# Kernel optimization log

Measured on AMD Instinct MI355X. Metric: run time of the kernel, lower is better.

## Reference

```python
import jax, jax.numpy as jnp
import numpy as np


def cv_sigmoid(z):
    # split sigmoid: sigmoid(Re) + i*sigmoid(Im)
    return jax.nn.sigmoid(z.real) + 1j * jax.nn.sigmoid(z.imag)


def cv_polar_tanh(z):
    # tanh on magnitude, phase preserved: tanh(|z|) * z / |z|
    mag = jnp.abs(z)
    safe = jnp.where(mag == 0, 1.0, mag)
    return (jnp.tanh(mag) / safe).astype(z.dtype) * z


def setup_inputs() -> dict:
    key = jax.random.key(0)
    B, D, H = 16384, 512, 512
    ks = jax.random.split(key, 12)
    names = ['x_re', 'x_im', 'h_re', 'h_im', 'Wx_re', 'Wx_im', 'Wh_re', 'Wh_im', 'bx_re', 'bx_im', 'bh_re', 'bh_im']
    shapes = [(B, D), (B, D), (B, H), (B, H), (3, H, D), (3, H, D), (3, H, H), (3, H, H), (3, H), (3, H), (3, H), (3, H)]
    out = {}
    for n, s, k in zip(names, shapes, ks):
        scale = 1.0 if n[0] in ('x', 'h') else (1.0 / np.sqrt(s[-1]))
        out[n] = jax.random.normal(k, s, dtype=jnp.float32) * scale
    return out


def reference(x_re, x_im, h_re, h_im, Wx_re, Wx_im, Wh_re, Wh_im, bx_re, bx_im, bh_re, bh_im):
    x = (x_re + 1j * x_im).astype(jnp.complex64)   # [B, D]
    h = (h_re + 1j * h_im).astype(jnp.complex64)   # [B, H]
    Wx = (Wx_re + 1j * Wx_im).astype(jnp.complex64)  # [3, H, D] (z, r, h)
    Wh = (Wh_re + 1j * Wh_im).astype(jnp.complex64)  # [3, H, H]
    bx = (bx_re + 1j * bx_im).astype(jnp.complex64)  # [3, H]
    bh = (bh_re + 1j * bh_im).astype(jnp.complex64)  # [3, H]

    # input projections for all three gates at once: [3, B, H]
    px = jnp.einsum('bd,khd->kbh', x, Wx) + bx[:, None, :]
    # hidden projections for z and r gates
    pz = jnp.einsum('bh,gh->bg', h, Wh[0]) + bh[0]
    pr = jnp.einsum('bh,gh->bg', h, Wh[1]) + bh[1]

    z = cv_sigmoid(px[0] + pz)
    r = cv_sigmoid(px[1] + pr)

    ph = jnp.einsum('bh,gh->bg', r * h, Wh[2]) + bh[2]
    h_tilde = cv_polar_tanh(px[2] + ph)

    h_new = (1.0 - z) * h + z * h_tilde  # [B, H] complex
    # return as stacked real/imag float tensor [B, H, 2]
    return jnp.stack([h_new.real, h_new.imag], axis=-1)
```

## Files before the change

### kernel.cpp

```cpp
#include <hip/hip_runtime.h>
#include <hip/hip_bf16.h>

typedef __bf16 bf16_t;
typedef __bf16 bf16x8 __attribute__((ext_vector_type(8)));
typedef __bf16 bf16x4 __attribute__((ext_vector_type(4)));
typedef float f32x4 __attribute__((ext_vector_type(4)));


__device__ __forceinline__ void gl_lds16(const bf16_t* g, bf16_t* l) {
  __builtin_amdgcn_global_load_lds(
      (const __attribute__((address_space(1))) void*)g,
      (__attribute__((address_space(3))) void*)l, 16, 0, 0);
}

__device__ __forceinline__ float fast_sigmoid(float x) {
  return 1.0f / (1.0f + __expf(-x));
}

__global__ void pack_A(const float* __restrict__ x_re, const float* __restrict__ x_im,
                       const float* __restrict__ h_re, const float* __restrict__ h_im,
                       bf16_t* __restrict__ A) {
  int q = blockIdx.x * blockDim.x + threadIdx.x;
  int i4 = q << 2;
  int b = i4 >> 11;
  int k = i4 & 2047;
  int seg = k >> 9;
  int off = k & 511;
  const float* s = (seg == 0) ? x_re : (seg == 1) ? x_im : (seg == 2) ? h_re : h_im;
  const float4 v = *(const float4*)(s + (size_t)b * 512 + off);
  bf16x4 o = { (bf16_t)v.x, (bf16_t)v.y, (bf16_t)v.z, (bf16_t)v.w };
  *(bf16x4*)(A + (size_t)b * 2048 + k) = o;
}

__global__ void pack_W(const float* __restrict__ Wx_re, const float* __restrict__ Wx_im,
                       const float* __restrict__ Wh_re, const float* __restrict__ Wh_im,
                       bf16_t* __restrict__ W1t, bf16_t* __restrict__ W2t) {
  int q = blockIdx.x * blockDim.x + threadIdx.x;
  int n, k2, g, j, p;
  const float *Wre, *Wim;
  bf16_t* dst;
  if (q < 1048576) {
    n = q >> 9; k2 = (q & 511) << 2;
    g = n >> 10; j = (n & 1023) >> 1; p = n & 1;
    int pair = k2 >> 10;
    Wre = pair ? Wh_re : Wx_re;
    Wim = pair ? Wh_im : Wx_im;
    dst = W1t + (size_t)n * 2048 + k2;
  } else if (q < 1048576 + 262144) {
    int q2 = q - 1048576;
    n = 2048 + (q2 >> 8); k2 = (q2 & 255) << 2;
    g = 2; j = (n - 2048) >> 1; p = n & 1;
    Wre = Wx_re; Wim = Wx_im;
    dst = W1t + (size_t)n * 2048 + k2;
  } else {
    int q3 = q - (1048576 + 262144);
    n = q3 >> 8; k2 = (q3 & 255) << 2;
    g = 2; j = n >> 1; p = n & 1;
    Wre = Wh_re; Wim = Wh_im;
    dst = W2t + (size_t)n * 1024 + k2;
  }
  int klocal = k2 & 1023;
  int half = klocal >> 9;
  int off = klocal & 511;
  size_t sidx = ((size_t)g * 512 + j) * 512 + off;
  const float* s = (half == 0) ? (p ? Wim : Wre) : (p ? Wre : Wim);
  float sgn = (half == 1 && p == 0) ? -1.0f : 1.0f;
  float4 v = *(const float4*)(s + sidx);
  bf16x4 o = { (bf16_t)(sgn * v.x), (bf16_t)(sgn * v.y),
               (bf16_t)(sgn * v.z), (bf16_t)(sgn * v.w) };
  *(bf16x4*)dst = o;
}

template <int MODE>
__launch_bounds__(512, 2)
__global__ void gemm_fused(const bf16_t* __restrict__ A, const bf16_t* __restrict__ W,
                           int LDA, int LDW,
                           bf16_t* __restrict__ zbuf, bf16_t* __restrict__ A2,
                           float* __restrict__ outbuf,
                           const float* __restrict__ h_re, const float* __restrict__ h_im,
                           const float* __restrict__ bx_re, const float* __restrict__ bx_im,
                           const float* __restrict__ bh_re, const float* __restrict__ bh_im) {
  __shared__ __align__(16) bf16_t As[2][256 * 64];
  __shared__ __align__(16) bf16_t Bs[2][256 * 64];

  const int bid = blockIdx.x;
  const int xcd = bid & 7;
  const int idx = bid >> 3;
  const int ntile = idx >> 3;
  const int mtile = (xcd << 3) + (idx & 7);
  const int m0 = mtile * 256;
  const int n0 = ntile * 256;
  const int region = (MODE == 1) ? (ntile >> 2) : 0;
  const int KEND = (MODE == 1) ? ((region < 2) ? 2048 : 1024) : 1024;
  const int nKT = KEND >> 6;

  const int tid = threadIdx.x;
  const int lane = tid & 63;
  const int w = tid >> 6;
  const int wr = w >> 2;
  const int wc = w & 3;

  const int rb = tid >> 3;
  const int cc = tid & 7;
  const int cs = cc ^ (rb & 7);
  const bf16_t* Ag = A + (size_t)(m0 + rb) * LDA + cs * 8;
  const bf16_t* Wg = W + (size_t)(n0 + rb) * LDW + cs * 8;

#define STAGE_A(s, bufi, kt2) \
  gl_lds16(Ag + (size_t)(s) * 64 * LDA + (kt2) * 64, &As[bufi][tid * 8 + (s) * 4096])
#define STAGE_B(s, bufi, kt2) \
  gl_lds16(Wg + (size_t)(s) * 64 * LDW + (kt2) * 64, &Bs[bufi][tid * 8 + (s) * 4096])

  const int quad = lane >> 4, lrow = lane & 15;
  int aOff[8], bOff[4];
#pragma unroll
  for (int mt = 0; mt < 8; ++mt) {
    const int r = wr * 128 + mt * 16 + lrow;
    aOff[mt] = r * 64 + ((quad ^ (r & 7)) << 3);
  }
#pragma unroll
  for (int nt = 0; nt < 4; ++nt) {
    const int r = wc * 64 + nt * 16 + lrow;
    bOff[nt] = r * 64 + ((quad ^ (r & 7)) << 3);
  }

  f32x4 acc[8][4] = {};

#pragma unroll
  for (int s = 0; s < 4; ++s) STAGE_A(s, 0, 0);
#pragma unroll
  for (int s = 0; s < 4; ++s) STAGE_B(s, 0, 0);
  STAGE_A(0, 1, 1);
  STAGE_A(2, 1, 1);
  asm volatile("s_waitcnt vmcnt(2)" ::: "memory");
  __builtin_amdgcn_s_barrier();

  for (int kt = 0; kt < nKT; ++kt) {
    const int b = kt & 1;
    const bf16_t* Ab = As[b];
    const bf16_t* Bb = Bs[b];
    const bool s1 = (kt + 1 < nKT);
    const bool s2 = (kt + 2 < nKT);

    bf16x8 bk0[4], bk1[4], aA[4], aB[4], aC[4], aD[4];

#pragma unroll
    for (int nt = 0; nt < 4; ++nt) bk0[nt] = *(const bf16x8*)(Bb + bOff[nt]);
#pragma unroll
    for (int i = 0; i < 4; ++i) aA[i] = *(const bf16x8*)(Ab + aOff[i]);
#pragma unroll
    for (int i = 0; i < 4; ++i) aB[i] = *(const bf16x8*)(Ab + aOff[4 + i]);
    if (s1) { STAGE_A(1, b ^ 1, kt + 1); STAGE_A(3, b ^ 1, kt + 1); }
    asm volatile("" ::: "memory");
    __builtin_amdgcn_s_barrier();
    __builtin_amdgcn_s_setprio(1);
#pragma unroll
    for (int i = 0; i < 4; ++i)
#pragma unroll
      for (int nt = 0; nt < 4; ++nt)
        acc[i][nt] = __builtin_amdgcn_mfma_f32_16x16x32_bf16(aA[i], bk0[nt], acc[i][nt], 0, 0, 0);
    __builtin_amdgcn_s_setprio(0);
    __builtin_amdgcn_s_barrier();

#pragma unroll
    for (int i = 0; i < 4; ++i) aC[i] = *(const bf16x8*)(Ab + (aOff[i] ^ 32));
#pragma unroll
    for (int nt = 0; nt < 4; ++nt) bk1[nt] = *(const bf16x8*)(Bb + (bOff[nt] ^ 32));
    if (s1) { STAGE_B(0, b ^ 1, kt + 1); STAGE_B(1, b ^ 1, kt + 1); }
    asm volatile("" ::: "memory");
    __builtin_amdgcn_s_barrier();
    __builtin_amdgcn_s_setprio(1);
#pragma unroll
    for (int i = 0; i < 4; ++i)
#pragma unroll
      for (int nt = 0; nt < 4; ++nt)
        acc[4 + i][nt] = __builtin_amdgcn_mfma_f32_16x16x32_bf16(aB[i], bk0[nt], acc[4 + i][nt], 0, 0, 0);
    __builtin_amdgcn_s_setprio(0);
    __builtin_amdgcn_s_barrier();

#pragma unroll
    for (int i = 0; i < 4; ++i) aD[i] = *(const bf16x8*)(Ab + (aOff[4 + i] ^ 32));
    if (s1) { STAGE_B(2, b ^ 1, kt + 1); STAGE_B(3, b ^ 1, kt + 1); }
    asm volatile("" ::: "memory");
    __builtin_amdgcn_s_barrier();
    __builtin_amdgcn_s_setprio(1);
#pragma unroll
    for (int i = 0; i < 4; ++i)
#pragma unroll
      for (int nt = 0; nt < 4; ++nt)
        acc[i][nt] = __builtin_amdgcn_mfma_f32_16x16x32_bf16(aC[i], bk1[nt], acc[i][nt], 0, 0, 0);
    __builtin_amdgcn_s_setprio(0);
    __builtin_amdgcn_s_barrier();

    if (s2) { STAGE_A(0, b, kt + 2); STAGE_A(2, b, kt + 2); }
    asm volatile("" ::: "memory");
    __builtin_amdgcn_s_barrier();
    __builtin_amdgcn_s_setprio(1);
#pragma unroll
    for (int i = 0; i < 4; ++i)
#pragma unroll
      for (int nt = 0; nt < 4; ++nt)
        acc[4 + i][nt] = __builtin_amdgcn_mfma_f32_16x16x32_bf16(aD[i], bk1[nt], acc[4 + i][nt], 0, 0, 0);
    __builtin_amdgcn_s_setprio(0);

    if (s1) {
      if (s2) asm volatile("s_waitcnt vmcnt(2)" ::: "memory");
      else    asm volatile("s_waitcnt vmcnt(0)" ::: "memory");
      __builtin_amdgcn_s_barrier();
    }
  }
#undef STAGE_A
#undef STAGE_B

#pragma unroll
  for (int mt = 0; mt < 8; ++mt) {
#pragma unroll
    for (int nt = 0; nt < 4; ++nt) {
#pragma unroll
      for (int rg = 0; rg < 4; ++rg) {
        const int m = m0 + wr * 128 + mt * 16 + quad * 4 + rg;
        const int n = n0 + wc * 64 + nt * 16 + lrow;
        float v = acc[mt][nt][rg];
        const int p = n & 1;

        if (MODE == 1) {
          const int cj = n & 1023;
          const int j = cj >> 1;
          const float bias = p ? (bx_im[region * 512 + j] + bh_im[region * 512 + j])
                               : (bx_re[region * 512 + j] + bh_re[region * 512 + j]);
          const float val = v + bias;
          if (region == 0) {
            zbuf[(size_t)m * 1024 + cj] = (bf16_t)fast_sigmoid(val);
          } else if (region == 1) {
            float rv = fast_sigmoid(val);
            float ro = __shfl_xor(rv, 1, 64);
            float hp = p ? h_im[(size_t)m * 512 + j] : h_re[(size_t)m * 512 + j];
            float ho = __shfl_xor(hp, 1, 64);
            float rh = (p == 0) ? (rv * hp - ro * ho) : (ro * hp + rv * ho);
            A2[(size_t)m * 1024 + p * 512 + j] = (bf16_t)rh;
          } else {
            outbuf[(size_t)m * 1024 + cj] = val;
          }
        } else {
          const int j = n >> 1;
          float tv = outbuf[(size_t)m * 1024 + n];
          float u = tv + v;
          float uo = __shfl_xor(u, 1, 64);
          float mag = sqrtf(u * u + uo * uo);
          float mm = fminf(mag, 20.0f);
          float e = __expf(2.0f * mm);
          float th = (e - 1.0f) / (e + 1.0f);
          float s = (mag == 0.0f) ? 0.0f : (th / mag);
          float hto = s * u;
          float htd = s * uo;
          float zv = (float)zbuf[(size_t)m * 1024 + n];
          float zo = __shfl_xor(zv, 1, 64);
          float hp = p ? h_im[(size_t)m * 512 + j] : h_re[(size_t)m * 512 + j];
          float ho = __shfl_xor(hp, 1, 64);
          float res;
          if (p == 0)
            res = (1.0f - zv) * hp + zo * ho + zv * hto - zo * htd;
          else
            res = (1.0f - zo) * hp - zv * ho + zo * hto + zv * htd;
          outbuf[(size_t)m * 1024 + n] = res;
        }
      }
    }
  }
}

extern "C" void kernel_launch(void* const* d_in, const int* in_sizes, int n_in,
                              void* d_out, int out_size, void* d_ws, size_t ws_size,
                              hipStream_t stream) {
  const float* x_re  = (const float*)d_in[0];
  const float* x_im  = (const float*)d_in[1];
  const float* h_re  = (const float*)d_in[2];
  const float* h_im  = (const float*)d_in[3];
  const float* Wx_re = (const float*)d_in[4];
  const float* Wx_im = (const float*)d_in[5];
  const float* Wh_re = (const float*)d_in[6];
  const float* Wh_im = (const float*)d_in[7];
  const float* bx_re = (const float*)d_in[8];
  const float* bx_im = (const float*)d_in[9];
  const float* bh_re = (const float*)d_in[10];
  const float* bh_im = (const float*)d_in[11];
  float* out = (float*)d_out;

  char* ws = (char*)d_ws;
  bf16_t* A_big = (bf16_t*)(ws);
  bf16_t* W1t   = (bf16_t*)(ws + 67108864);
  bf16_t* W2t   = (bf16_t*)(ws + 79691776);
  bf16_t* A2    = (bf16_t*)(ws + 81788928);
  bf16_t* zbuf  = (bf16_t*)(ws + 115343360);

  pack_A<<<32768, 256, 0, stream>>>(x_re, x_im, h_re, h_im, A_big);
  pack_W<<<6144, 256, 0, stream>>>(Wx_re, Wx_im, Wh_re, Wh_im, W1t, W2t);
  gemm_fused<1><<<768, 512, 0, stream>>>(A_big, W1t, 2048, 2048,
      zbuf, A2, out, h_re, h_im, bx_re, bx_im, bh_re, bh_im);
  gemm_fused<2><<<256, 512, 0, stream>>>(A2, W2t, 1024, 1024,
      zbuf, A2, out, h_re, h_im, bx_re, bx_im, bh_re, bh_im);
}
```

Measured before the change: 639.0 us.

## Restructure GEMM main loop prefetch schedule to single-stage lookahead with fewer registers

Reorders the global-to-LDS staging so that the next k-tile's B and A halves are issued during the current tile's four MFMA phases, replacing the earlier scheme that prefetched A two tiles ahead. The fragment registers are reduced from six sets to three reused sets, and explicit lgkmcnt and vmcnt waits are placed per phase. This lowers register pressure and simplifies the pipeline. It trades away prefetch depth, which may expose more global-load latency.

```diff
diff --git a/kernel.cpp b/kernel.cpp
--- a/kernel.cpp
+++ b/kernel.cpp
@@ -126,12 +126,9 @@
 
   f32x4 acc[8][4] = {};
 
-#pragma unroll
-  for (int s = 0; s < 4; ++s) STAGE_A(s, 0, 0);
-#pragma unroll
-  for (int s = 0; s < 4; ++s) STAGE_B(s, 0, 0);
-  STAGE_A(0, 1, 1);
-  STAGE_A(2, 1, 1);
+  STAGE_B(0, 0, 0); STAGE_B(1, 0, 0); STAGE_B(2, 0, 0); STAGE_B(3, 0, 0);
+  STAGE_A(0, 0, 0); STAGE_A(2, 0, 0);
+  STAGE_A(1, 0, 0); STAGE_A(3, 0, 0);
   asm volatile("s_waitcnt vmcnt(2)" ::: "memory");
   __builtin_amdgcn_s_barrier();
 
@@ -140,74 +137,71 @@
     const bf16_t* Ab = As[b];
     const bf16_t* Bb = Bs[b];
     const bool s1 = (kt + 1 < nKT);
-    const bool s2 = (kt + 2 < nKT);
-
-    bf16x8 bk0[4], bk1[4], aA[4], aB[4], aC[4], aD[4];
-
-#pragma unroll
-    for (int nt = 0; nt < 4; ++nt) bk0[nt] = *(const bf16x8*)(Bb + bOff[nt]);
-#pragma unroll
-    for (int i = 0; i < 4; ++i) aA[i] = *(const bf16x8*)(Ab + aOff[i]);
-#pragma unroll
-    for (int i = 0; i < 4; ++i) aB[i] = *(const bf16x8*)(Ab + aOff[4 + i]);
+
+    bf16x8 bk[4], bk1[4], af[4];
+
+#pragma unroll
+    for (int nt = 0; nt < 4; ++nt) bk[nt] = *(const bf16x8*)(Bb + bOff[nt]);
+#pragma unroll
+    for (int i = 0; i < 4; ++i) af[i] = *(const bf16x8*)(Ab + aOff[i]);
+    if (s1) { STAGE_B(0, b ^ 1, kt + 1); STAGE_B(1, b ^ 1, kt + 1); }
+    __builtin_amdgcn_s_barrier();
+    asm volatile("s_waitcnt lgkmcnt(0)" ::: "memory");
+    __builtin_amdgcn_s_setprio(1);
+#pragma unroll
+    for (int i = 0; i < 4; ++i)
+#pragma unroll
+      for (int nt = 0; nt < 4; ++nt)
+        acc[i][nt] = __builtin_amdgcn_mfma_f32_16x16x32_bf16(af[i], bk[nt], acc[i][nt], 0, 0, 0);
+    __builtin_amdgcn_s_setprio(0);
+    if (s1) asm volatile("s_waitcnt vmcnt(2)" ::: "memory");
+    else    asm volatile("s_waitcnt vmcnt(0)" ::: "memory");
+    __builtin_amdgcn_s_barrier();
+
+#pragma unroll
+    for (int i = 0; i < 4; ++i) af[i] = *(const bf16x8*)(Ab + aOff[4 + i]);
+    if (s1) { STAGE_B(2, b ^ 1, kt + 1); STAGE_B(3, b ^ 1, kt + 1); }
+    __builtin_amdgcn_s_barrier();
+    asm volatile("s_waitcnt lgkmcnt(0)" ::: "memory");
+    __builtin_amdgcn_s_setprio(1);
+#pragma unroll
+    for (int i = 0; i < 4; ++i)
+#pragma unroll
+      for (int nt = 0; nt < 4; ++nt)
+        acc[4 + i][nt] = __builtin_amdgcn_mfma_f32_16x16x32_bf16(af[i], bk[nt], acc[4 + i][nt], 0, 0, 0);
+    __builtin_amdgcn_s_setprio(0);
+    __builtin_amdgcn_s_barrier();
+
+#pragma unroll
+    for (int nt = 0; nt < 4; ++nt) bk1[nt] = *(const bf16x8*)(Bb + (bOff[nt] ^ 32));
+#pragma unroll
+    for (int i = 0; i < 4; ++i) af[i] = *(const bf16x8*)(Ab + (aOff[i] ^ 32));
+    if (s1) { STAGE_A(0, b ^ 1, kt + 1); STAGE_A(2, b ^ 1, kt + 1); }
+    __builtin_amdgcn_s_barrier();
+    asm volatile("s_waitcnt lgkmcnt(0)" ::: "memory");
+    __builtin_amdgcn_s_setprio(1);
+#pragma unroll
+    for (int i = 0; i < 4; ++i)
+#pragma unroll
+      for (int nt = 0; nt < 4; ++nt)
+        acc[i][nt] = __builtin_amdgcn_mfma_f32_16x16x32_bf16(af[i], bk1[nt], acc[i][nt], 0, 0, 0);
+    __builtin_amdgcn_s_setprio(0);
+    __builtin_amdgcn_s_barrier();
+
+#pragma unroll
+    for (int i = 0; i < 4; ++i) af[i] = *(const bf16x8*)(Ab + (aOff[4 + i] ^ 32));
     if (s1) { STAGE_A(1, b ^ 1, kt + 1); STAGE_A(3, b ^ 1, kt + 1); }
-    asm volatile("" ::: "memory");
-    __builtin_amdgcn_s_barrier();
-    __builtin_amdgcn_s_setprio(1);
-#pragma unroll
-    for (int i = 0; i < 4; ++i)
-#pragma unroll
-      for (int nt = 0; nt < 4; ++nt)
-        acc[i][nt] = __builtin_amdgcn_mfma_f32_16x16x32_bf16(aA[i], bk0[nt], acc[i][nt], 0, 0, 0);
-    __builtin_amdgcn_s_setprio(0);
-    __builtin_amdgcn_s_barrier();
-
-#pragma unroll
-    for (int i = 0; i < 4; ++i) aC[i] = *(const bf16x8*)(Ab + (aOff[i] ^ 32));
-#pragma unroll
-    for (int nt = 0; nt < 4; ++nt) bk1[nt] = *(const bf16x8*)(Bb + (bOff[nt] ^ 32));
-    if (s1) { STAGE_B(0, b ^ 1, kt + 1); STAGE_B(1, b ^ 1, kt + 1); }
-    asm volatile("" ::: "memory");
-    __builtin_amdgcn_s_barrier();
-    __builtin_amdgcn_s_setprio(1);
-#pragma unroll
-    for (int i = 0; i < 4; ++i)
-#pragma unroll
-      for (int nt = 0; nt < 4; ++nt)
-        acc[4 + i][nt] = __builtin_amdgcn_mfma_f32_16x16x32_bf16(aB[i], bk0[nt], acc[4 + i][nt], 0, 0, 0);
-    __builtin_amdgcn_s_setprio(0);
-    __builtin_amdgcn_s_barrier();
-
-#pragma unroll
-    for (int i = 0; i < 4; ++i) aD[i] = *(const bf16x8*)(Ab + (aOff[4 + i] ^ 32));
-    if (s1) { STAGE_B(2, b ^ 1, kt + 1); STAGE_B(3, b ^ 1, kt + 1); }
-    asm volatile("" ::: "memory");
-    __builtin_amdgcn_s_barrier();
-    __builtin_amdgcn_s_setprio(1);
-#pragma unroll
-    for (int i = 0; i < 4; ++i)
-#pragma unroll
-      for (int nt = 0; nt < 4; ++nt)
-        acc[i][nt] = __builtin_amdgcn_mfma_f32_16x16x32_bf16(aC[i], bk1[nt], acc[i][nt], 0, 0, 0);
-    __builtin_amdgcn_s_setprio(0);
-    __builtin_amdgcn_s_barrier();
-
-    if (s2) { STAGE_A(0, b, kt + 2); STAGE_A(2, b, kt + 2); }
-    asm volatile("" ::: "memory");
-    __builtin_amdgcn_s_barrier();
-    __builtin_amdgcn_s_setprio(1);
-#pragma unroll
-    for (int i = 0; i < 4; ++i)
-#pragma unroll
-      for (int nt = 0; nt < 4; ++nt)
-        acc[4 + i][nt] = __builtin_amdgcn_mfma_f32_16x16x32_bf16(aD[i], bk1[nt], acc[4 + i][nt], 0, 0, 0);
-    __builtin_amdgcn_s_setprio(0);
-
-    if (s1) {
-      if (s2) asm volatile("s_waitcnt vmcnt(2)" ::: "memory");
-      else    asm volatile("s_waitcnt vmcnt(0)" ::: "memory");
-      __builtin_amdgcn_s_barrier();
-    }
+    __builtin_amdgcn_s_barrier();
+    asm volatile("s_waitcnt lgkmcnt(0)" ::: "memory");
+    __builtin_amdgcn_s_setprio(1);
+#pragma unroll
+    for (int i = 0; i < 4; ++i)
+#pragma unroll
+      for (int nt = 0; nt < 4; ++nt)
+        acc[4 + i][nt] = __builtin_amdgcn_mfma_f32_16x16x32_bf16(af[i], bk1[nt], acc[4 + i][nt], 0, 0, 0);
+    __builtin_amdgcn_s_setprio(0);
+    if (s1) asm volatile("s_waitcnt vmcnt(2)" ::: "memory");
+    __builtin_amdgcn_s_barrier();
   }
 #undef STAGE_A
 #undef STAGE_B
```

New measurement: 645.6 us. About the same (+1.0%).
